# Optimization experiments

Hardware: AMD Instinct MI355X
Metric: run time of the kernel (lower is better)

The kernel has to match this reference:

```python
import jax, jax.numpy as jnp
import numpy as np

N, E, D, H = 50000, 800000, 128, 8
C = D // H  # head dim = 16

def _layer_norm(x, g, b, eps=1e-5):
    mu = jnp.mean(x, axis=-1, keepdims=True)
    var = jnp.var(x, axis=-1, keepdims=True)
    return (x - mu) * jax.lax.rsqrt(var + eps) * g + b

def setup_inputs() -> dict:
    key = jax.random.key(0)
    ks = jax.random.split(key, 24)
    def lin(i, fan_in=D):
        s = 1.0 / np.sqrt(fan_in)
        return (jax.random.uniform(ks[i], (D, D), minval=-s, maxval=s),
                jax.random.uniform(ks[i + 1], (D,), minval=-s, maxval=s))
    Wq, bq = lin(0); Wk, bk = lin(2); Wv, bv = lin(4)
    We, be = lin(6); Ws, bs = lin(8)
    W1, b1 = lin(10); W2, b2 = lin(12)
    return {
        'edge_index': jax.random.randint(ks[14], (2, E), 0, N),
        'node_attr': jax.random.normal(ks[15], (N, D), dtype=jnp.float32),
        'edge_attr': jax.random.normal(ks[16], (E, D), dtype=jnp.float32),
        'Wq': Wq, 'bq': bq, 'Wk': Wk, 'bk': bk, 'Wv': Wv, 'bv': bv,
        'We': We, 'be': be, 'Ws': Ws, 'bs': bs,
        'W1': W1, 'b1': b1, 'W2': W2, 'b2': b2,
        'ln1_g': jnp.ones((D,)), 'ln1_b': jnp.zeros((D,)),
        'ln2_g': jnp.ones((D,)), 'ln2_b': jnp.zeros((D,)),
    }

def _transformer_conv(node_attr, edge_attr, src, dst, Wq, bq, Wk, bk, Wv, bv, We, be, Ws, bs):
    # PyG TransformerConv, concat=True, root_weight=True, beta=False, eval (no dropout)
    q = (node_attr @ Wq.T + bq).reshape(N, H, C)[dst]          # [E,H,C]
    e = (edge_attr @ We.T + be).reshape(E, H, C)               # [E,H,C]
    k = (node_attr @ Wk.T + bk).reshape(N, H, C)[src] + e      # [E,H,C]
    v = (node_attr @ Wv.T + bv).reshape(N, H, C)[src] + e      # [E,H,C]
    alpha = jnp.sum(q * k, axis=-1) / jnp.sqrt(jnp.float32(C)) # [E,H]
    # segment softmax over destination node
    m = jax.ops.segment_max(alpha, dst, num_segments=N)        # [N,H]
    ex = jnp.exp(alpha - m[dst])
    denom = jax.ops.segment_sum(ex, dst, num_segments=N)       # [N,H]
    a = ex / (denom[dst] + 1e-16)                              # [E,H]
    out = jax.ops.segment_sum(v * a[..., None], dst, num_segments=N)  # [N,H,C]
    out = out.reshape(N, D)
    return out + node_attr @ Ws.T + bs  # root/skip connection

def reference(edge_index, node_attr, edge_attr, Wq, bq, Wk, bk, Wv, bv, We, be,
              Ws, bs, W1, b1, W2, b2, ln1_g, ln1_b, ln2_g, ln2_b):
    src, dst = edge_index[0], edge_index[1]
    x = _transformer_conv(node_attr, edge_attr, src, dst,
                          Wq, bq, Wk, bk, Wv, bv, We, be, Ws, bs)
    node_attr = node_attr + _layer_norm(x, ln1_g, ln1_b)
    h = jax.nn.silu(node_attr @ W1.T + b1) @ W2.T + b2
    node_attr = node_attr + _layer_norm(h, ln2_g, ln2_b)
    return node_attr
```

## Files before the change

### kernel.cpp

```cpp
#include <hip/hip_runtime.h>
#include <hip/hip_fp16.h>

#define N_NODES 50000
#define N_EDGES 800000
#define DIM 128
#define NODE_TILES 782
#define EDGE_TILES 12500
#define EDGE_BLOCKS 2500
#define SCAN_NB 50

typedef _Float16 f16;
typedef _Float16 f16x2 __attribute__((ext_vector_type(2)));
typedef _Float16 f16x4 __attribute__((ext_vector_type(4)));
typedef _Float16 f16x8 __attribute__((ext_vector_type(8)));
typedef float    f32x16 __attribute__((ext_vector_type(16)));

__device__ __forceinline__ void sfence() { __builtin_amdgcn_sched_barrier(0); }

__device__ __forceinline__ void load_wfrag(const f16* __restrict__ Wh, int ch, int l31, int g,
                                           f16x8 bf[2][8]) {
#pragma unroll
  for (int c = 0; c < 2; ++c)
#pragma unroll
    for (int ks = 0; ks < 8; ++ks)
      bf[c][ks] = *(const f16x8*)(Wh + ((ch * 64 + c * 32 + l31) << 7) + 16 * ks + 8 * g);
}

template <int HALF_OUT, int SILU>
__device__ __forceinline__ void gemm_store(f32x16 acc[2], long M, const float* __restrict__ Bv,
                                           void* __restrict__ OUT,
                                           long tile0, int rc, int ch, int l31, int g) {
#pragma unroll
  for (int c = 0; c < 2; ++c) {
    int col = ch * 64 + c * 32 + l31;
    float bv = Bv[col];
#pragma unroll
    for (int r = 0; r < 16; ++r) {
      long gm = tile0 + rc * 32 + ((r & 3) + 8 * (r >> 2) + 4 * g);
      if (gm < M) {
        float v = acc[c][r] + bv;
        if (SILU) v = v / (1.0f + __expf(-v));
        if (HALF_OUT) ((f16*)OUT)[gm * DIM + col] = (f16)v;
        else          ((float*)OUT)[gm * DIM + col] = v;
      }
    }
  }
}

__device__ __forceinline__ void stage_issue(const float* __restrict__ X, long M, long base,
                                            int tid, float4 sv[8]) {
#pragma unroll
  for (int kk = 0; kk < 8; ++kk) {
    int i = tid + kk * 256;
    long row = base + (i >> 5);
    long gr = row < M ? row : (M - 1);
    sv[kk] = *(const float4*)(X + gr * DIM + (i & 31) * 4);
  }
}

__device__ __forceinline__ void stage_issue_g(const float* __restrict__ X,
                                              const int* __restrict__ elist, long base,
                                              int tid, float4 sv[8]) {
#pragma unroll
  for (int kk = 0; kk < 8; ++kk) {
    int i = tid + kk * 256;
    int eid = elist[base + (i >> 5)];
    sv[kk] = *(const float4*)(X + (long)eid * DIM + (i & 31) * 4);
  }
}

__device__ __forceinline__ void stage_write(const float4 sv[8], int tid, f16* __restrict__ lds) {
#pragma unroll
  for (int kk = 0; kk < 8; ++kk) {
    int i = tid + kk * 256;
    int r = i >> 5, s8 = i & 31;
    f16x4 h;
    h[0] = (f16)sv[kk].x; h[1] = (f16)sv[kk].y; h[2] = (f16)sv[kk].z; h[3] = (f16)sv[kk].w;
    *(f16x4*)(lds + r * 128 + (((s8 >> 1) ^ (r & 15)) << 3) + ((s8 & 1) << 2)) = h;
  }
}

__device__ __forceinline__ void mfma_lds_g(const f16* __restrict__ A, int lr, int g,
                                           const f16x8 bf[2][8], f32x16 acc[2]) {
#pragma unroll
  for (int c = 0; c < 2; ++c)
#pragma unroll
    for (int k = 0; k < 16; ++k) acc[c][k] = 0.0f;
#pragma unroll
  for (int ks = 0; ks < 8; ++ks) {
    f16x8 a = *(const f16x8*)(A + lr * 128 + (((2 * ks + g) ^ (lr & 15)) << 3));
    acc[0] = __builtin_amdgcn_mfma_f32_32x32x16_f16(a, bf[0][ks], acc[0], 0, 0, 0);
    acc[1] = __builtin_amdgcn_mfma_f32_32x32x16_f16(a, bf[1][ks], acc[1], 0, 0, 0);
  }
}

__global__ __launch_bounds__(256) void big_gemms(const float* __restrict__ X,
    const float* __restrict__ EA, const int* __restrict__ elist,
    const f16* __restrict__ WhAll,
    const float* __restrict__ bq, const float* __restrict__ bk,
    const float* __restrict__ bv_, const float* __restrict__ bs, const float* __restrict__ be,
    f16* __restrict__ Q, f16* __restrict__ K, f16* __restrict__ V, float* __restrict__ S,
    f16* __restrict__ emat) {
  __shared__ f16 lbuf[2][64 * 128];
  int tid = threadIdx.x;
  int lane = tid & 63, w = tid >> 6;
  int rc = w >> 1, ch = w & 1, l31 = lane & 31, g = lane >> 5;
  int lr = rc * 32 + l31;

  if (blockIdx.x < NODE_TILES) {
    f16* xs = lbuf[0];
    long tile0 = (long)blockIdx.x * 64;
    float4 sv[8];
    stage_issue(X, N_NODES, tile0, tid, sv);
    stage_write(sv, tid, xs);
    __syncthreads();
#pragma unroll 1
    for (int mat = 0; mat < 4; ++mat) {
      f16x8 bf[2][8];
      load_wfrag(WhAll + mat * 16384, ch, l31, g, bf);
      f32x16 acc[2];
      mfma_lds_g(xs, lr, g, bf, acc);
      if (mat == 0)      gemm_store<1, 0>(acc, N_NODES, bq, Q, tile0, rc, ch, l31, g);
      else if (mat == 1) gemm_store<1, 0>(acc, N_NODES, bk, K, tile0, rc, ch, l31, g);
      else if (mat == 2) gemm_store<1, 0>(acc, N_NODES, bv_, V, tile0, rc, ch, l31, g);
      else               gemm_store<0, 0>(acc, N_NODES, bs, S, tile0, rc, ch, l31, g);
    }
    return;
  }

  int t0 = blockIdx.x - NODE_TILES;
  f16x8 bf[2][8];
  load_wfrag(WhAll + 4 * 16384, ch, l31, g, bf);
  float4 sv[8];
  stage_issue_g(EA, elist, (long)t0 * 64, tid, sv);
  stage_write(sv, tid, lbuf[0]);
  __syncthreads();
  int cur = 0;
  for (int t = t0; t < EDGE_TILES; t += EDGE_BLOCKS) {
    int tn = t + EDGE_BLOCKS;
    if (tn < EDGE_TILES) stage_issue_g(EA, elist, (long)tn * 64, tid, sv);
    sfence();
    f32x16 acc[2];
    mfma_lds_g(lbuf[cur], lr, g, bf, acc);
    gemm_store<1, 0>(acc, (long)N_EDGES, be, emat, (long)t * 64, rc, ch, l31, g);
    if (tn < EDGE_TILES) {
      asm volatile("s_waitcnt vmcnt(0)" ::: "memory");
      stage_write(sv, tid, lbuf[cur ^ 1]);
    }
    __syncthreads();
    cur ^= 1;
  }
}

__global__ __launch_bounds__(256) void mlp_ln(const float* __restrict__ X,
    const f16* __restrict__ W1h, const float* __restrict__ b1,
    const f16* __restrict__ W2h, const float* __restrict__ b2,
    const float* __restrict__ gv, const float* __restrict__ bv,
    float* __restrict__ outp) {
  __shared__ float smem[64 * 128];
  f16* xs = (f16*)smem;
  f16* hs = (f16*)smem + 64 * 128;
  float* wbuf = smem;
  int tid = threadIdx.x;
  int lane = tid & 63, w = tid >> 6;
  int rc = w >> 1, ch = w & 1, l31 = lane & 31, g = lane >> 5;
  int t = blockIdx.x;
  if (t >= NODE_TILES) return;
  long tile0 = (long)t * 64;
  int lr = rc * 32 + l31;

  float4 sv[8];
  stage_issue(X, N_NODES, tile0, tid, sv);
  f16x8 bf1[2][8];
  load_wfrag(W1h, ch, l31, g, bf1);
  stage_write(sv, tid, xs);
  __syncthreads();

  f32x16 acc[2];
  mfma_lds_g(xs, lr, g, bf1, acc);
  f16x8 bf2[2][8];
  load_wfrag(W2h, ch, l31, g, bf2);

#pragma unroll
  for (int c = 0; c < 2; ++c) {
    int col = ch * 64 + c * 32 + l31;
    float bb = b1[col];
#pragma unroll
    for (int r = 0; r < 16; ++r) {
      int row = rc * 32 + (r & 3) + 8 * (r >> 2) + 4 * g;
      float v = acc[c][r] + bb;
      v = v / (1.0f + __expf(-v));
      hs[row * 128 + (((col >> 3) ^ (row & 15)) << 3) + (col & 7)] = (f16)v;
    }
  }
  __syncthreads();

  f32x16 a2[2];
  mfma_lds_g(hs, lr, g, bf2, a2);
  __syncthreads();

#pragma unroll
  for (int c = 0; c < 2; ++c) {
    int col = ch * 64 + c * 32 + l31;
    float bb = b2[col];
#pragma unroll
    for (int r = 0; r < 16; ++r) {
      int row = rc * 32 + (r & 3) + 8 * (r >> 2) + 4 * g;
      wbuf[row * 128 + col] = a2[c][r] + bb;
    }
  }
  __syncthreads();

  float2 gg = *(const float2*)(gv + 2 * lane);
  float2 bb2 = *(const float2*)(bv + 2 * lane);
#pragma unroll 1
  for (int rr = 0; rr < 16; ++rr) {
    int row = w * 16 + rr;
    long gm = tile0 + row;
    if (gm >= N_NODES) break;
    float2 x;
    x.x = wbuf[row * 128 + 2 * lane];
    x.y = wbuf[row * 128 + 2 * lane + 1];
    float sm = x.x + x.y;
    for (int m = 1; m < 64; m <<= 1) sm += __shfl_xor(sm, m);
    float mu = sm * (1.f / 128.f);
    float dx = x.x - mu, dy = x.y - mu;
    float ss = dx * dx + dy * dy;
    for (int m = 1; m < 64; m <<= 1) ss += __shfl_xor(ss, m);
    float r = rsqrtf(ss * (1.f / 128.f) + 1e-5f);
    float2 bs = *(const float2*)(X + gm * DIM + 2 * lane);
    float2 o;
    o.x = bs.x + dx * r * gg.x + bb2.x;
    o.y = bs.y + dy * r * gg.y + bb2.y;
    *(float2*)(outp + gm * DIM + 2 * lane) = o;
  }
}

__global__ void hist_conv_k(const int* __restrict__ ei, int* __restrict__ counts,
                            const float* __restrict__ a0, const float* __restrict__ a1,
                            const float* __restrict__ a2, const float* __restrict__ a3,
                            const float* __restrict__ a4, const float* __restrict__ a5,
                            const float* __restrict__ a6, f16* __restrict__ dst) {
  long gid = blockIdx.x * 256L + threadIdx.x;
  if (gid < 7 * 16384) {
    int mat = (int)(gid >> 14), el = (int)(gid & 16383);
    const float* s = (mat == 0) ? a0 : (mat == 1) ? a1 : (mat == 2) ? a2 : (mat == 3) ? a3
                   : (mat == 4) ? a4 : (mat == 5) ? a5 : a6;
    dst[gid] = (f16)s[el];
  }
  for (long e = gid; e < N_EDGES; e += 1024L * 256)
    atomicAdd(&counts[ei[N_EDGES + e]], 1);
}

__global__ __launch_bounds__(1024) void blocksum_k(const int* __restrict__ counts,
                                                   int* __restrict__ bsum) {
  __shared__ int sd[1024];
  int t = threadIdx.x, b = blockIdx.x;
  int v = (t < 1000) ? counts[b * 1000 + t] : 0;
  sd[t] = v; __syncthreads();
  for (int off = 512; off > 0; off >>= 1) {
    if (t < off) sd[t] += sd[t + off];
    __syncthreads();
  }
  if (t == 0) bsum[b] = sd[0];
}

__global__ void scan_small(const int* __restrict__ bsum, int* __restrict__ boff,
                           int* __restrict__ offs) {
  if (threadIdx.x == 0) {
    int run = 0;
    for (int b = 0; b < SCAN_NB; ++b) { boff[b] = run; run += bsum[b]; }
    boff[SCAN_NB] = run;
    offs[N_NODES] = run;
  }
}

__global__ __launch_bounds__(1024) void expand_k(const int* __restrict__ counts,
                                                 const int* __restrict__ boff,
                                                 int* __restrict__ offs, int* __restrict__ cursor) {
  __shared__ int sd[1024];
  int t = threadIdx.x, b = blockIdx.x;
  int v = (t < 1000) ? counts[b * 1000 + t] : 0;
  sd[t] = v; __syncthreads();
  for (int off = 1; off < 1024; off <<= 1) {
    int x = (t >= off) ? sd[t - off] : 0;
    __syncthreads();
    sd[t] += x;
    __syncthreads();
  }
  if (t < 1000) {
    int o = boff[b] + sd[t] - v;
    int idx = b * 1000 + t;
    offs[idx] = o;
    cursor[idx] = o;
  }
}

__global__ void scatter_k(const int* __restrict__ ei, int* __restrict__ cursor,
                          int* __restrict__ elist, int* __restrict__ srcs) {
  for (long e = blockIdx.x * (long)blockDim.x + threadIdx.x; e < N_EDGES;
       e += (long)gridDim.x * blockDim.x) {
    int d = ei[N_EDGES + e];
    int pos = atomicAdd(&cursor[d], 1);
    elist[pos] = (int)e;
    srcs[pos] = ei[e];
  }
}

__global__ __launch_bounds__(256) void attn_ln(const int* __restrict__ offs,
    const int* __restrict__ srcs, const f16* __restrict__ emat, const f16* __restrict__ Qn,
    const f16* __restrict__ Kn, const f16* __restrict__ Vn,
    const float* __restrict__ Skip, const float* __restrict__ base,
    const float* __restrict__ gv, const float* __restrict__ bv,
    float* __restrict__ outp) {
  int n = blockIdx.x * 4 + (threadIdx.x >> 6);
  if (n >= N_NODES) return;
  int lane = threadIdx.x & 63;
  int grp = lane >> 4, li = lane & 15;
  int c8 = 8 * li;

  float q[8];
  {
    f16x8 qv = *(const f16x8*)(Qn + (long)n * DIM + c8);
#pragma unroll
    for (int k = 0; k < 8; ++k) q[k] = (float)qv[k];
  }

  int rs = offs[n], re = offs[n + 1];
  float a[8];
#pragma unroll
  for (int k = 0; k < 8; ++k) a[k] = 0.f;
  float den = 0.f;

  if (rs < re) {
    int e0 = rs + grp;
    int sCur = srcs[(e0 < re) ? e0 : (re - 1)];
    for (int i = rs; i < re; i += 4) {
      int ei_ = i + grp;
      bool valid = ei_ < re;
      int ec = valid ? ei_ : (re - 1);
      int s = sCur;
      int en = ei_ + 4;
      sCur = srcs[(en < re) ? en : (re - 1)];
      f16x8 e8 = *(const f16x8*)(emat + (long)ec * DIM + c8);
      f16x8 k8 = *(const f16x8*)(Kn + (long)s * DIM + c8);
      f16x8 v8 = *(const f16x8*)(Vn + (long)s * DIM + c8);
      float p = 0.f;
#pragma unroll
      for (int k = 0; k < 8; ++k) p += q[k] * ((float)k8[k] + (float)e8[k]);
      p += __shfl_xor(p, 1);
      float ex = valid ? __expf(p * 0.25f) : 0.f;
      den += ex;
#pragma unroll
      for (int k = 0; k < 8; ++k) a[k] += ex * ((float)e8[k] + (float)v8[k]);
    }
  }
#pragma unroll
  for (int k = 0; k < 8; ++k) {
    a[k] += __shfl_xor(a[k], 16);
    a[k] += __shfl_xor(a[k], 32);
  }
  den += __shfl_xor(den, 16);
  den += __shfl_xor(den, 32);

  float inv = 1.f / (den + 1e-16f);
  float x[8];
  {
    float4 sk0 = *(const float4*)(Skip + (long)n * DIM + c8);
    float4 sk1 = *(const float4*)(Skip + (long)n * DIM + c8 + 4);
    x[0] = a[0] * inv + sk0.x; x[1] = a[1] * inv + sk0.y;
    x[2] = a[2] * inv + sk0.z; x[3] = a[3] * inv + sk0.w;
    x[4] = a[4] * inv + sk1.x; x[5] = a[5] * inv + sk1.y;
    x[6] = a[6] * inv + sk1.z; x[7] = a[7] * inv + sk1.w;
  }

  float sm = 0.f;
#pragma unroll
  for (int k = 0; k < 8; ++k) sm += x[k];
  for (int m = 1; m < 16; m <<= 1) sm += __shfl_xor(sm, m);
  float mu = sm * (1.f / 128.f);
  float d[8], ss = 0.f;
#pragma unroll
  for (int k = 0; k < 8; ++k) { d[k] = x[k] - mu; ss += d[k] * d[k]; }
  for (int m = 1; m < 16; m <<= 1) ss += __shfl_xor(ss, m);
  float r = rsqrtf(ss * (1.f / 128.f) + 1e-5f);

  if (grp == 0) {
    float4 g0 = *(const float4*)(gv + c8);
    float4 g1 = *(const float4*)(gv + c8 + 4);
    float4 b0 = *(const float4*)(bv + c8);
    float4 b1 = *(const float4*)(bv + c8 + 4);
    float4 s0 = *(const float4*)(base + (long)n * DIM + c8);
    float4 s1 = *(const float4*)(base + (long)n * DIM + c8 + 4);
    float4 o0, o1;
    o0.x = s0.x + d[0] * r * g0.x + b0.x;
    o0.y = s0.y + d[1] * r * g0.y + b0.y;
    o0.z = s0.z + d[2] * r * g0.z + b0.z;
    o0.w = s0.w + d[3] * r * g0.w + b0.w;
    o1.x = s1.x + d[4] * r * g1.x + b1.x;
    o1.y = s1.y + d[5] * r * g1.y + b1.y;
    o1.z = s1.z + d[6] * r * g1.z + b1.z;
    o1.w = s1.w + d[7] * r * g1.w + b1.w;
    *(float4*)(outp + (long)n * DIM + c8) = o0;
    *(float4*)(outp + (long)n * DIM + c8 + 4) = o1;
  }
}

extern "C" void kernel_launch(void* const* d_in, const int* in_sizes, int n_in,
                              void* d_out, int out_size, void* d_ws, size_t ws_size,
                              hipStream_t stream) {
  (void)in_sizes; (void)n_in; (void)out_size; (void)ws_size;
  const int*   ei  = (const int*)d_in[0];
  const float* x0  = (const float*)d_in[1];
  const float* ea  = (const float*)d_in[2];
  const float* Wq  = (const float*)d_in[3];  const float* bq = (const float*)d_in[4];
  const float* Wk  = (const float*)d_in[5];  const float* bk = (const float*)d_in[6];
  const float* Wv  = (const float*)d_in[7];  const float* bv = (const float*)d_in[8];
  const float* We  = (const float*)d_in[9];  const float* be = (const float*)d_in[10];
  const float* Wsk = (const float*)d_in[11]; const float* bsk = (const float*)d_in[12];
  const float* W1  = (const float*)d_in[13]; const float* b1 = (const float*)d_in[14];
  const float* W2  = (const float*)d_in[15]; const float* b2 = (const float*)d_in[16];
  const float* g1  = (const float*)d_in[17]; const float* lb1 = (const float*)d_in[18];
  const float* g2  = (const float*)d_in[19]; const float* lb2 = (const float*)d_in[20];

  char* ws = (char*)d_ws;
  f16*   Qn     = (f16*)(ws + 0);
  f16*   Kn     = (f16*)(ws + 12800000L);
  f16*   Vn     = (f16*)(ws + 25600000L);
  float* Skip   = (float*)(ws + 38400000L);
  int*   offs   = (int*)(ws + 64000000L);
  f16*   WhAll  = (f16*)(ws + 64200192L);
  int*   cursor = (int*)(ws + 64200192L);
  int*   counts = (int*)(ws + 64429568L);
  int*   bsum   = (int*)(ws + 64629760L);
  int*   boff   = bsum + 64;
  int*   elist  = (int*)(ws + 64630272L);
  int*   srcs   = (int*)(ws + 67830272L);
  f16*   emat   = (f16*)(ws + 71030272L);
  float* node1  = (float*)(ws + 275830272L);

  f16* WhAll2 = (f16*)(ws + 301430272L);

  (void)hipMemsetAsync(counts, 0, N_NODES * sizeof(int), stream);
  hist_conv_k<<<1024, 256, 0, stream>>>(ei, counts, Wq, Wk, Wv, Wsk, We, W1, W2, WhAll2);
  blocksum_k<<<SCAN_NB, 1024, 0, stream>>>(counts, bsum);
  scan_small<<<1, 64, 0, stream>>>(bsum, boff, offs);
  expand_k<<<SCAN_NB, 1024, 0, stream>>>(counts, boff, offs, cursor);
  scatter_k<<<1024, 256, 0, stream>>>(ei, cursor, elist, srcs);

  big_gemms<<<NODE_TILES + EDGE_BLOCKS, 256, 0, stream>>>(
      x0, ea, elist, WhAll2, bq, bk, bv, bsk, be, Qn, Kn, Vn, Skip, emat);
  attn_ln<<<12500, 256, 0, stream>>>(offs, srcs, emat, Qn, Kn, Vn, Skip, x0, g1, lb1, node1);
  mlp_ln<<<NODE_TILES, 256, 0, stream>>>(node1, WhAll2 + 5 * 16384, b1,
                                         WhAll2 + 6 * 16384, b2, g2, lb2, (float*)d_out);
}
```

Before: 471.8 us.

## Replace persistent double-buffered edge GEMM loop with one tile per block

The edge-attribute GEMM part of big_gemms previously used 2500 persistent blocks, each looping over five tiles with a double-buffered LDS prefetch. Now each of 12500 blocks handles a single 64-edge tile with one LDS buffer. That halves shared memory per block, which can raise occupancy, and removes the loop and buffer-swap logic. In exchange, every block reloads the We weight fragments and there is no explicit load/compute overlap inside a block; the scheduler has to hide latency across blocks instead. The unused aliased WhAll pointer is also cleaned up.

```diff
diff --git a/kernel.cpp b/kernel.cpp
--- a/kernel.cpp
+++ b/kernel.cpp
@@ -6,7 +6,6 @@
 #define DIM 128
 #define NODE_TILES 782
 #define EDGE_TILES 12500
-#define EDGE_BLOCKS 2500
 #define SCAN_NB 50
 
 typedef _Float16 f16;
@@ -101,25 +100,24 @@
     const float* __restrict__ bv_, const float* __restrict__ bs, const float* __restrict__ be,
     f16* __restrict__ Q, f16* __restrict__ K, f16* __restrict__ V, float* __restrict__ S,
     f16* __restrict__ emat) {
-  __shared__ f16 lbuf[2][64 * 128];
+  __shared__ f16 lbuf[64 * 128];
   int tid = threadIdx.x;
   int lane = tid & 63, w = tid >> 6;
   int rc = w >> 1, ch = w & 1, l31 = lane & 31, g = lane >> 5;
   int lr = rc * 32 + l31;
 
   if (blockIdx.x < NODE_TILES) {
-    f16* xs = lbuf[0];
     long tile0 = (long)blockIdx.x * 64;
     float4 sv[8];
     stage_issue(X, N_NODES, tile0, tid, sv);
-    stage_write(sv, tid, xs);
+    stage_write(sv, tid, lbuf);
     __syncthreads();
 #pragma unroll 1
     for (int mat = 0; mat < 4; ++mat) {
       f16x8 bf[2][8];
       load_wfrag(WhAll + mat * 16384, ch, l31, g, bf);
       f32x16 acc[2];
-      mfma_lds_g(xs, lr, g, bf, acc);
+      mfma_lds_g(lbuf, lr, g, bf, acc);
       if (mat == 0)      gemm_store<1, 0>(acc, N_NODES, bq, Q, tile0, rc, ch, l31, g);
       else if (mat == 1) gemm_store<1, 0>(acc, N_NODES, bk, K, tile0, rc, ch, l31, g);
       else if (mat == 2) gemm_store<1, 0>(acc, N_NODES, bv_, V, tile0, rc, ch, l31, g);
@@ -128,28 +126,17 @@
     return;
   }
 
-  int t0 = blockIdx.x - NODE_TILES;
+  long tile0 = (long)(blockIdx.x - NODE_TILES) * 64;
+  float4 sv[8];
+  stage_issue_g(EA, elist, tile0, tid, sv);
+  sfence();
+  stage_write(sv, tid, lbuf);
+  __syncthreads();
   f16x8 bf[2][8];
   load_wfrag(WhAll + 4 * 16384, ch, l31, g, bf);
-  float4 sv[8];
-  stage_issue_g(EA, elist, (long)t0 * 64, tid, sv);
-  stage_write(sv, tid, lbuf[0]);
-  __syncthreads();
-  int cur = 0;
-  for (int t = t0; t < EDGE_TILES; t += EDGE_BLOCKS) {
-    int tn = t + EDGE_BLOCKS;
-    if (tn < EDGE_TILES) stage_issue_g(EA, elist, (long)tn * 64, tid, sv);
-    sfence();
-    f32x16 acc[2];
-    mfma_lds_g(lbuf[cur], lr, g, bf, acc);
-    gemm_store<1, 0>(acc, (long)N_EDGES, be, emat, (long)t * 64, rc, ch, l31, g);
-    if (tn < EDGE_TILES) {
-      asm volatile("s_waitcnt vmcnt(0)" ::: "memory");
-      stage_write(sv, tid, lbuf[cur ^ 1]);
-    }
-    __syncthreads();
-    cur ^= 1;
-  }
+  f32x16 acc[2];
+  mfma_lds_g(lbuf, lr, g, bf, acc);
+  gemm_store<1, 0>(acc, (long)N_EDGES, be, emat, tile0, rc, ch, l31, g);
 }
 
 __global__ __launch_bounds__(256) void mlp_ln(const float* __restrict__ X,
@@ -429,7 +416,6 @@
   f16*   Vn     = (f16*)(ws + 25600000L);
   float* Skip   = (float*)(ws + 38400000L);
   int*   offs   = (int*)(ws + 64000000L);
-  f16*   WhAll  = (f16*)(ws + 64200192L);
   int*   cursor = (int*)(ws + 64200192L);
   int*   counts = (int*)(ws + 64429568L);
   int*   bsum   = (int*)(ws + 64629760L);
@@ -438,19 +424,18 @@
   int*   srcs   = (int*)(ws + 67830272L);
   f16*   emat   = (f16*)(ws + 71030272L);
   float* node1  = (float*)(ws + 275830272L);
-
-  f16* WhAll2 = (f16*)(ws + 301430272L);
+  f16*   WhAll  = (f16*)(ws + 301430272L);
 
   (void)hipMemsetAsync(counts, 0, N_NODES * sizeof(int), stream);
-  hist_conv_k<<<1024, 256, 0, stream>>>(ei, counts, Wq, Wk, Wv, Wsk, We, W1, W2, WhAll2);
+  hist_conv_k<<<1024, 256, 0, stream>>>(ei, counts, Wq, Wk, Wv, Wsk, We, W1, W2, WhAll);
   blocksum_k<<<SCAN_NB, 1024, 0, stream>>>(counts, bsum);
   scan_small<<<1, 64, 0, stream>>>(bsum, boff, offs);
   expand_k<<<SCAN_NB, 1024, 0, stream>>>(counts, boff, offs, cursor);
   scatter_k<<<1024, 256, 0, stream>>>(ei, cursor, elist, srcs);
 
-  big_gemms<<<NODE_TILES + EDGE_BLOCKS, 256, 0, stream>>>(
-      x0, ea, elist, WhAll2, bq, bk, bv, bsk, be, Qn, Kn, Vn, Skip, emat);
+  big_gemms<<<NODE_TILES + EDGE_TILES, 256, 0, stream>>>(
+      x0, ea, elist, WhAll, bq, bk, bv, bsk, be, Qn, Kn, Vn, Skip, emat);
   attn_ln<<<12500, 256, 0, stream>>>(offs, srcs, emat, Qn, Kn, Vn, Skip, x0, g1, lb1, node1);
-  mlp_ln<<<NODE_TILES, 256, 0, stream>>>(node1, WhAll2 + 5 * 16384, b1,
-                                         WhAll2 + 6 * 16384, b2, g2, lb2, (float*)d_out);
-}
+  mlp_ln<<<NODE_TILES, 256, 0, stream>>>(node1, WhAll + 5 * 16384, b1,
+                                         WhAll + 6 * 16384, b2, g2, lb2, (float*)d_out);
+}
```

Measured after the change: 469.5 us. About the same (-0.5%).
